# Kernel optimization log

Hardware: AMD Instinct MI355X
Metric: run time of the kernel (lower is better)

## Reference

```python
import jax, jax.numpy as jnp
import numpy as np

D_MODEL = 768
N_HEAD = 12
D_K = D_MODEL // N_HEAD


def setup_inputs() -> dict:
    key = jax.random.key(0)
    ks = jax.random.split(key, 11)
    B, S = 2, 2048
    s = 1.0 / np.sqrt(D_MODEL)
    return {
        "q": jax.random.normal(ks[0], (B, S, D_MODEL), jnp.float32),
        "k": jax.random.normal(ks[1], (B, S, D_MODEL), jnp.float32),
        "v": jax.random.normal(ks[2], (B, S, D_MODEL), jnp.float32),
        "w_q": jax.random.normal(ks[3], (D_MODEL, D_MODEL), jnp.float32) * s,
        "b_q": jnp.zeros((D_MODEL,), jnp.float32),
        "w_k": jax.random.normal(ks[4], (D_MODEL, D_MODEL), jnp.float32) * s,
        "b_k": jnp.zeros((D_MODEL,), jnp.float32),
        "w_v": jax.random.normal(ks[5], (D_MODEL, D_MODEL), jnp.float32) * s,
        "b_v": jnp.zeros((D_MODEL,), jnp.float32),
        "w_o": jax.random.normal(ks[6], (D_MODEL, D_MODEL), jnp.float32) * s,
        "b_o": jnp.zeros((D_MODEL,), jnp.float32),
    }


def reference(q, k, v, w_q, b_q, w_k, b_k, w_v, b_v, w_o, b_o):
    B, S, _ = q.shape
    # QKV projections (nn.Linear: x @ W.T + b)
    Q = q @ w_q.T + b_q
    K = k @ w_k.T + b_k
    V = v @ w_v.T + b_v
    # [B, S, H, d_k] -> [B, H, S, d_k]
    Q = Q.reshape(B, S, N_HEAD, D_K).transpose(0, 2, 1, 3)
    K = K.reshape(B, S, N_HEAD, D_K).transpose(0, 2, 1, 3)
    V = V.reshape(B, S, N_HEAD, D_K).transpose(0, 2, 1, 3)
    # scaled dot-product attention, full [B, H, S, S] scores (as in source)
    scores = jnp.einsum('bhqd,bhkd->bhqk', Q, K) / jnp.sqrt(
        jnp.asarray(D_K, jnp.float32))
    attn = jax.nn.softmax(scores, axis=-1)
    x = jnp.einsum('bhqk,bhkd->bhqd', attn, V)
    x = x.transpose(0, 2, 1, 3).reshape(B, S, D_MODEL)
    out = x @ w_o.T + b_o
    return out, attn
```

## Files before the change

kernel.cpp:

```cpp
#include <hip/hip_runtime.h>

#define DM 768
#define SL 2048
#define NB 2
#define NH 12
#define DK 64

typedef __bf16 bf16x8 __attribute__((ext_vector_type(8)));
typedef float f32x4 __attribute__((ext_vector_type(4)));

__device__ __forceinline__ float bf2f(unsigned short u) {
  return __uint_as_float(((unsigned int)u) << 16);
}
__device__ __forceinline__ unsigned short f2bf(float f) {
  unsigned int u = __float_as_uint(f);
  u += 0x7fff + ((u >> 16) & 1);
  return (unsigned short)(u >> 16);
}

template <int AM, int BM, int OM>
__global__ __launch_bounds__(256) void gemm_bt_t(
    const void* __restrict__ Av, int lda, long sAb, long sAh,
    const void* __restrict__ Bv, int ldb, long sBb, long sBh,
    void* __restrict__ Cv, void* __restrict__ Cv2, int ldc, long sCb, long sCh,
    const float* __restrict__ bias, float scale, int K, int zdiv) {
  constexpr bool SPLIT = (AM == 2);
  const int z = blockIdx.z, zb = z / zdiv, zh = z % zdiv;
  const long aoff = (long)zb * sAb + (long)zh * sAh;
  const long boff = (long)zb * sBb + (long)zh * sBh;
  const long coff = (long)zb * sCb + (long)zh * sCh;
  const int tm = blockIdx.y * 64, tn = blockIdx.x * 64;
  __shared__ __align__(16) unsigned short As[64][40];
  __shared__ __align__(16) unsigned short Bs[64][40];
  __shared__ __align__(16) unsigned short Al[SPLIT ? 64 : 1][40];
  __shared__ __align__(16) unsigned short Bl[SPLIT ? 64 : 1][40];
  const int tid = threadIdx.x;
  const int lrow = tid >> 2, lcol = (tid & 3) * 8;
  const int lane = tid & 63, wave = tid >> 6;
  const int wm = (wave >> 1) * 32, wn = (wave & 1) * 32;
  const int fr = lane & 15, quad = lane >> 4;
  f32x4 acc[2][2] = {};
  for (int k0 = 0; k0 < K; k0 += 32) {
    if constexpr (AM == 0) {
      const unsigned short* Ab = (const unsigned short*)Av + aoff;
      *(uint4*)&As[lrow][lcol] = *(const uint4*)(Ab + (long)(tm + lrow) * lda + k0 + lcol);
    } else {
      const float* Af = (const float*)Av + aoff + (long)(tm + lrow) * lda + k0 + lcol;
      float4 f0 = *(const float4*)Af;
      float4 f1 = *(const float4*)(Af + 4);
      float ff[8] = {f0.x, f0.y, f0.z, f0.w, f1.x, f1.y, f1.z, f1.w};
      unsigned short hi[8];
#pragma unroll
      for (int i = 0; i < 8; ++i) hi[i] = f2bf(ff[i]);
      *(uint4*)&As[lrow][lcol] = *(const uint4*)hi;
      if constexpr (SPLIT) {
        unsigned short lo[8];
#pragma unroll
        for (int i = 0; i < 8; ++i) lo[i] = f2bf(ff[i] - bf2f(hi[i]));
        *(uint4*)&Al[lrow][lcol] = *(const uint4*)lo;
      }
    }
    if constexpr (BM == 0) {
      const unsigned short* Bb = (const unsigned short*)Bv + boff;
      *(uint4*)&Bs[lrow][lcol] = *(const uint4*)(Bb + (long)(tn + lrow) * ldb + k0 + lcol);
    } else {
      const float* Bf = (const float*)Bv + boff + (long)(tn + lrow) * ldb + k0 + lcol;
      float4 f0 = *(const float4*)Bf;
      float4 f1 = *(const float4*)(Bf + 4);
      float ff[8] = {f0.x, f0.y, f0.z, f0.w, f1.x, f1.y, f1.z, f1.w};
      unsigned short hi[8];
#pragma unroll
      for (int i = 0; i < 8; ++i) hi[i] = f2bf(ff[i]);
      *(uint4*)&Bs[lrow][lcol] = *(const uint4*)hi;
      if constexpr (SPLIT) {
        unsigned short lo[8];
#pragma unroll
        for (int i = 0; i < 8; ++i) lo[i] = f2bf(ff[i] - bf2f(hi[i]));
        *(uint4*)&Bl[lrow][lcol] = *(const uint4*)lo;
      }
    }
    __syncthreads();
    bf16x8 a0 = *(const bf16x8*)&As[wm + fr][quad * 8];
    bf16x8 a1 = *(const bf16x8*)&As[wm + 16 + fr][quad * 8];
    bf16x8 b0 = *(const bf16x8*)&Bs[wn + fr][quad * 8];
    bf16x8 b1 = *(const bf16x8*)&Bs[wn + 16 + fr][quad * 8];
    acc[0][0] = __builtin_amdgcn_mfma_f32_16x16x32_bf16(a0, b0, acc[0][0], 0, 0, 0);
    acc[0][1] = __builtin_amdgcn_mfma_f32_16x16x32_bf16(a0, b1, acc[0][1], 0, 0, 0);
    acc[1][0] = __builtin_amdgcn_mfma_f32_16x16x32_bf16(a1, b0, acc[1][0], 0, 0, 0);
    acc[1][1] = __builtin_amdgcn_mfma_f32_16x16x32_bf16(a1, b1, acc[1][1], 0, 0, 0);
    if constexpr (SPLIT) {
      bf16x8 c0 = *(const bf16x8*)&Al[wm + fr][quad * 8];
      bf16x8 c1 = *(const bf16x8*)&Al[wm + 16 + fr][quad * 8];
      bf16x8 d0 = *(const bf16x8*)&Bl[wn + fr][quad * 8];
      bf16x8 d1 = *(const bf16x8*)&Bl[wn + 16 + fr][quad * 8];
      acc[0][0] = __builtin_amdgcn_mfma_f32_16x16x32_bf16(c0, b0, acc[0][0], 0, 0, 0);
      acc[0][1] = __builtin_amdgcn_mfma_f32_16x16x32_bf16(c0, b1, acc[0][1], 0, 0, 0);
      acc[1][0] = __builtin_amdgcn_mfma_f32_16x16x32_bf16(c1, b0, acc[1][0], 0, 0, 0);
      acc[1][1] = __builtin_amdgcn_mfma_f32_16x16x32_bf16(c1, b1, acc[1][1], 0, 0, 0);
      acc[0][0] = __builtin_amdgcn_mfma_f32_16x16x32_bf16(a0, d0, acc[0][0], 0, 0, 0);
      acc[0][1] = __builtin_amdgcn_mfma_f32_16x16x32_bf16(a0, d1, acc[0][1], 0, 0, 0);
      acc[1][0] = __builtin_amdgcn_mfma_f32_16x16x32_bf16(a1, d0, acc[1][0], 0, 0, 0);
      acc[1][1] = __builtin_amdgcn_mfma_f32_16x16x32_bf16(a1, d1, acc[1][1], 0, 0, 0);
    }
    __syncthreads();
  }
#pragma unroll
  for (int sm = 0; sm < 2; ++sm)
#pragma unroll
    for (int sn = 0; sn < 2; ++sn) {
      const int gcol = tn + wn + sn * 16 + fr;
      const float bv = bias ? bias[gcol] : 0.0f;
#pragma unroll
      for (int r = 0; r < 4; ++r) {
        const int grow = tm + wm + sm * 16 + quad * 4 + r;
        const float val = acc[sm][sn][r] * scale + bv;
        const long ci = coff + (long)grow * ldc + gcol;
        if constexpr (OM == 1) {
          ((float*)Cv)[ci] = val;
        } else if constexpr (OM == 0) {
          ((unsigned short*)Cv)[ci] = f2bf(val);
        } else {
          const unsigned short hi = f2bf(val);
          ((unsigned short*)Cv)[ci] = hi;
          ((unsigned short*)Cv2)[ci] = f2bf(val - bf2f(hi));
        }
      }
    }
}

__global__ __launch_bounds__(256) void attn_fused(
    const unsigned short* __restrict__ Qh, const unsigned short* __restrict__ Ql,
    const unsigned short* __restrict__ Kh, const unsigned short* __restrict__ Kl,
    const unsigned short* __restrict__ Vb,
    float* __restrict__ attn, unsigned short* __restrict__ Xb) {
  const int bid = blockIdx.x;
  const int swz = (bid & 7) * 96 + (bid >> 3);
  const int rb = swz & 31;
  const int bh = swz >> 5;
  const int zb = bh / NH, zh = bh - zb * NH;
  const long qoff = (long)zb * SL * DM + zh * DK;
  const unsigned short* Qhb = Qh + qoff;
  const unsigned short* Qlb = Ql + qoff;
  const unsigned short* Khb = Kh + qoff;
  const unsigned short* Klb = Kl + qoff;
  const unsigned short* Vbb = Vb + qoff;
  float* attnb = attn + (long)bh * SL * SL;
  unsigned short* Xbb = Xb + qoff;

  __shared__ __align__(16) unsigned short KhS[64][72];
  __shared__ __align__(16) unsigned short KlS[64][72];
  __shared__ __align__(16) unsigned short VtS[64][72];
  __shared__ __align__(16) float PF[4][16][68];

  const int tid = threadIdx.x;
  const int lane = tid & 63, w = tid >> 6;
  const int fr = lane & 15, quad = lane >> 4;
  const int srow = tid >> 3, scol = (tid & 7) * 8;
  const int row0 = rb * 64 + w * 16;

  bf16x8 qh[2], ql[2];
#pragma unroll
  for (int kc = 0; kc < 2; ++kc) {
    uint4 hv = *(const uint4*)(Qhb + (long)(row0 + fr) * DM + kc * 32 + quad * 8);
    uint4 lv = *(const uint4*)(Qlb + (long)(row0 + fr) * DM + kc * 32 + quad * 8);
    const unsigned short* hp = (const unsigned short*)&hv;
    const unsigned short* lp = (const unsigned short*)&lv;
    unsigned short hs[8], ls[8];
#pragma unroll
    for (int i = 0; i < 8; ++i) {
      hs[i] = f2bf(bf2f(hp[i]) * 0.125f);
      ls[i] = f2bf(bf2f(lp[i]) * 0.125f);
    }
    qh[kc] = *(const bf16x8*)hs;
    ql[kc] = *(const bf16x8*)ls;
  }

  float lsum[4] = {0.0f, 0.0f, 0.0f, 0.0f};

  for (int kt = 0; kt < 32; ++kt) {
#pragma unroll
    for (int hf = 0; hf < 2; ++hf) {
      const int r0 = srow + hf * 32;
      const long g = (long)(kt * 64 + r0) * DM + scol;
      *(uint4*)&KhS[r0][scol] = *(const uint4*)(Khb + g);
      *(uint4*)&KlS[r0][scol] = *(const uint4*)(Klb + g);
    }
    __syncthreads();
    f32x4 s[4] = {};
    __builtin_amdgcn_s_setprio(1);
#pragma unroll
    for (int kc = 0; kc < 2; ++kc)
#pragma unroll
      for (int nf = 0; nf < 4; ++nf) {
        bf16x8 kh_ = *(const bf16x8*)&KhS[nf * 16 + fr][kc * 32 + quad * 8];
        bf16x8 kl_ = *(const bf16x8*)&KlS[nf * 16 + fr][kc * 32 + quad * 8];
        s[nf] = __builtin_amdgcn_mfma_f32_16x16x32_bf16(qh[kc], kh_, s[nf], 0, 0, 0);
        s[nf] = __builtin_amdgcn_mfma_f32_16x16x32_bf16(ql[kc], kh_, s[nf], 0, 0, 0);
        s[nf] = __builtin_amdgcn_mfma_f32_16x16x32_bf16(qh[kc], kl_, s[nf], 0, 0, 0);
      }
    __builtin_amdgcn_s_setprio(0);
#pragma unroll
    for (int nf = 0; nf < 4; ++nf)
#pragma unroll
      for (int r = 0; r < 4; ++r) lsum[r] += __expf(s[nf][r]);
    __syncthreads();
  }
#pragma unroll
  for (int r = 0; r < 4; ++r) {
#pragma unroll
    for (int off = 8; off; off >>= 1) lsum[r] += __shfl_xor(lsum[r], off, 64);
  }
  float inv[4];
#pragma unroll
  for (int r = 0; r < 4; ++r) inv[r] = 1.0f / lsum[r];

  f32x4 o[4] = {};
  for (int kt = 0; kt < 32; ++kt) {
    const int cx = tid & 7;
#pragma unroll
    for (int hf = 0; hf < 2; ++hf) {
      const int r0 = srow + hf * 32;
      const long g = (long)(kt * 64 + r0) * DM + scol;
      *(uint4*)&KhS[r0][scol] = *(const uint4*)(Khb + g);
      *(uint4*)&KlS[r0][scol] = *(const uint4*)(Klb + g);
      uint4 vv = *(const uint4*)(Vbb + g);
      const unsigned short* vp = (const unsigned short*)&vv;
#pragma unroll
      for (int i = 0; i < 8; ++i) {
        const int ii = i ^ (r0 & 7) ^ cx;
        VtS[scol + ii][r0] = vp[ii];
      }
    }
    __syncthreads();
    f32x4 s[4] = {};
    __builtin_amdgcn_s_setprio(1);
#pragma unroll
    for (int kc = 0; kc < 2; ++kc)
#pragma unroll
      for (int nf = 0; nf < 4; ++nf) {
        bf16x8 kh_ = *(const bf16x8*)&KhS[nf * 16 + fr][kc * 32 + quad * 8];
        bf16x8 kl_ = *(const bf16x8*)&KlS[nf * 16 + fr][kc * 32 + quad * 8];
        s[nf] = __builtin_amdgcn_mfma_f32_16x16x32_bf16(qh[kc], kh_, s[nf], 0, 0, 0);
        s[nf] = __builtin_amdgcn_mfma_f32_16x16x32_bf16(ql[kc], kh_, s[nf], 0, 0, 0);
        s[nf] = __builtin_amdgcn_mfma_f32_16x16x32_bf16(qh[kc], kl_, s[nf], 0, 0, 0);
      }
    __builtin_amdgcn_s_setprio(0);
#pragma unroll
    for (int nf = 0; nf < 4; ++nf)
#pragma unroll
      for (int r = 0; r < 4; ++r)
        PF[w][quad * 4 + r][nf * 16 + fr] = __expf(s[nf][r]) * inv[r];
    {
      const int lr = lane >> 2, lc = (lane & 3) * 16;
      float* dst = &attnb[(long)(row0 + lr) * SL + kt * 64 + lc];
      const float* src = &PF[w][lr][lc];
#pragma unroll
      for (int j = 0; j < 4; ++j)
        *(float4*)(dst + j * 4) = *(const float4*)(src + j * 4);
    }
    __builtin_amdgcn_s_setprio(1);
#pragma unroll
    for (int kc = 0; kc < 2; ++kc) {
      const float* pf = &PF[w][fr][kc * 32 + quad * 8];
      float4 p0 = *(const float4*)pf;
      float4 p1 = *(const float4*)(pf + 4);
      union { bf16x8 v; __bf16 e[8]; } pa;
      pa.e[0] = (__bf16)p0.x; pa.e[1] = (__bf16)p0.y;
      pa.e[2] = (__bf16)p0.z; pa.e[3] = (__bf16)p0.w;
      pa.e[4] = (__bf16)p1.x; pa.e[5] = (__bf16)p1.y;
      pa.e[6] = (__bf16)p1.z; pa.e[7] = (__bf16)p1.w;
#pragma unroll
      for (int nf = 0; nf < 4; ++nf) {
        bf16x8 vb_ = *(const bf16x8*)&VtS[nf * 16 + fr][kc * 32 + quad * 8];
        o[nf] = __builtin_amdgcn_mfma_f32_16x16x32_bf16(pa.v, vb_, o[nf], 0, 0, 0);
      }
    }
    __builtin_amdgcn_s_setprio(0);
    __syncthreads();
  }
#pragma unroll
  for (int nf = 0; nf < 4; ++nf)
#pragma unroll
    for (int r = 0; r < 4; ++r)
      Xbb[(long)(row0 + quad * 4 + r) * DM + nf * 16 + fr] = f2bf(o[nf][r]);
}

extern "C" void kernel_launch(void* const* d_in, const int* in_sizes, int n_in,
                              void* d_out, int out_size, void* d_ws, size_t ws_size,
                              hipStream_t stream) {
  const float* q  = (const float*)d_in[0];
  const float* k  = (const float*)d_in[1];
  const float* v  = (const float*)d_in[2];
  const float* wq = (const float*)d_in[3];
  const float* bq = (const float*)d_in[4];
  const float* wk = (const float*)d_in[5];
  const float* bk = (const float*)d_in[6];
  const float* wv = (const float*)d_in[7];
  const float* bv = (const float*)d_in[8];
  const float* wo = (const float*)d_in[9];
  const float* bo = (const float*)d_in[10];

  float* out  = (float*)d_out;
  float* attn = out + (long)NB * SL * DM;

  const long NE = (long)NB * SL * DM;
  unsigned short* Qh = (unsigned short*)d_ws;
  unsigned short* Ql = Qh + NE;
  unsigned short* Kh = Ql + NE;
  unsigned short* Kl = Kh + NE;
  unsigned short* Vbk = Kl + NE;
  unsigned short* Xb = Vbk + NE;

  const dim3 blk(256);
  const dim3 gp(DM / 64, (NB * SL) / 64, 1);

  gemm_bt_t<2, 2, 2><<<gp, blk, 0, stream>>>(q, DM, 0L, 0L, wq, DM, 0L, 0L,
                                             Qh, Ql, DM, 0L, 0L, bq, 1.0f, DM, 1);
  gemm_bt_t<2, 2, 2><<<gp, blk, 0, stream>>>(k, DM, 0L, 0L, wk, DM, 0L, 0L,
                                             Kh, Kl, DM, 0L, 0L, bk, 1.0f, DM, 1);
  gemm_bt_t<1, 1, 0><<<gp, blk, 0, stream>>>(v, DM, 0L, 0L, wv, DM, 0L, 0L,
                                             Vbk, nullptr, DM, 0L, 0L, bv, 1.0f, DM, 1);

  attn_fused<<<dim3((NB * NH * SL) / 64), blk, 0, stream>>>(Qh, Ql, Kh, Kl, Vbk,
                                                            attn, Xb);

  gemm_bt_t<0, 1, 1><<<gp, blk, 0, stream>>>(Xb, DM, 0L, 0L, wo, DM, 0L, 0L,
                                             out, nullptr, DM, 0L, 0L, bo, 1.0f, DM, 1);
}
```

Measured before the change: 716.2 us.

## Compute transposed scores to keep P in registers and drop LDS staging

Swaps the MFMA operand order so each lane holds one query row's scores across keys. Row sums then reduce with two cross-quad shuffles instead of per-row 16-lane reductions. The probability tile no longer round-trips through the PF shared buffer: attn is written directly with float4 stores, and the bf16 A-operand for the PV MFMA is built with packed converts plus permlane swaps. This removes LDS traffic and shared memory use, which may raise occupancy, but relies on gfx950 permlane semantics and changes the global store pattern for attn.

Result: faster. 675.2 us (-5.7%).

```diff
diff --git a/kernel.cpp b/kernel.cpp
--- a/kernel.cpp
+++ b/kernel.cpp
@@ -16,6 +16,11 @@
   unsigned int u = __float_as_uint(f);
   u += 0x7fff + ((u >> 16) & 1);
   return (unsigned short)(u >> 16);
+}
+__device__ __forceinline__ unsigned cvt_pk_bf16(float lo, float hi) {
+  unsigned r;
+  asm("v_cvt_pk_bf16_f32 %0, %1, %2" : "=v"(r) : "v"(lo), "v"(hi));
+  return r;
 }
 
 template <int AM, int BM, int OM>
@@ -150,7 +155,6 @@
   __shared__ __align__(16) unsigned short KhS[64][72];
   __shared__ __align__(16) unsigned short KlS[64][72];
   __shared__ __align__(16) unsigned short VtS[64][72];
-  __shared__ __align__(16) float PF[4][16][68];
 
   const int tid = threadIdx.x;
   const int lane = tid & 63, w = tid >> 6;
@@ -175,7 +179,7 @@
     ql[kc] = *(const bf16x8*)ls;
   }
 
-  float lsum[4] = {0.0f, 0.0f, 0.0f, 0.0f};
+  float lsum = 0.0f;
 
   for (int kt = 0; kt < 32; ++kt) {
 #pragma unroll
@@ -194,25 +198,23 @@
       for (int nf = 0; nf < 4; ++nf) {
         bf16x8 kh_ = *(const bf16x8*)&KhS[nf * 16 + fr][kc * 32 + quad * 8];
         bf16x8 kl_ = *(const bf16x8*)&KlS[nf * 16 + fr][kc * 32 + quad * 8];
-        s[nf] = __builtin_amdgcn_mfma_f32_16x16x32_bf16(qh[kc], kh_, s[nf], 0, 0, 0);
-        s[nf] = __builtin_amdgcn_mfma_f32_16x16x32_bf16(ql[kc], kh_, s[nf], 0, 0, 0);
-        s[nf] = __builtin_amdgcn_mfma_f32_16x16x32_bf16(qh[kc], kl_, s[nf], 0, 0, 0);
+        s[nf] = __builtin_amdgcn_mfma_f32_16x16x32_bf16(kh_, qh[kc], s[nf], 0, 0, 0);
+        s[nf] = __builtin_amdgcn_mfma_f32_16x16x32_bf16(kh_, ql[kc], s[nf], 0, 0, 0);
+        s[nf] = __builtin_amdgcn_mfma_f32_16x16x32_bf16(kl_, qh[kc], s[nf], 0, 0, 0);
       }
     __builtin_amdgcn_s_setprio(0);
-#pragma unroll
-    for (int nf = 0; nf < 4; ++nf)
-#pragma unroll
-      for (int r = 0; r < 4; ++r) lsum[r] += __expf(s[nf][r]);
+    float p0 = 0.0f, p1 = 0.0f, p2 = 0.0f, p3 = 0.0f;
+#pragma unroll
+    for (int nf = 0; nf < 4; ++nf) {
+      p0 += __expf(s[nf][0]); p1 += __expf(s[nf][1]);
+      p2 += __expf(s[nf][2]); p3 += __expf(s[nf][3]);
+    }
+    lsum += (p0 + p1) + (p2 + p3);
     __syncthreads();
   }
-#pragma unroll
-  for (int r = 0; r < 4; ++r) {
-#pragma unroll
-    for (int off = 8; off; off >>= 1) lsum[r] += __shfl_xor(lsum[r], off, 64);
-  }
-  float inv[4];
-#pragma unroll
-  for (int r = 0; r < 4; ++r) inv[r] = 1.0f / lsum[r];
+  lsum += __shfl_xor(lsum, 16, 64);
+  lsum += __shfl_xor(lsum, 32, 64);
+  const float inv = 1.0f / lsum;
 
   f32x4 o[4] = {};
   for (int kt = 0; kt < 32; ++kt) {
@@ -240,42 +242,41 @@
       for (int nf = 0; nf < 4; ++nf) {
         bf16x8 kh_ = *(const bf16x8*)&KhS[nf * 16 + fr][kc * 32 + quad * 8];
         bf16x8 kl_ = *(const bf16x8*)&KlS[nf * 16 + fr][kc * 32 + quad * 8];
-        s[nf] = __builtin_amdgcn_mfma_f32_16x16x32_bf16(qh[kc], kh_, s[nf], 0, 0, 0);
-        s[nf] = __builtin_amdgcn_mfma_f32_16x16x32_bf16(ql[kc], kh_, s[nf], 0, 0, 0);
-        s[nf] = __builtin_amdgcn_mfma_f32_16x16x32_bf16(qh[kc], kl_, s[nf], 0, 0, 0);
+        s[nf] = __builtin_amdgcn_mfma_f32_16x16x32_bf16(kh_, qh[kc], s[nf], 0, 0, 0);
+        s[nf] = __builtin_amdgcn_mfma_f32_16x16x32_bf16(kh_, ql[kc], s[nf], 0, 0, 0);
+        s[nf] = __builtin_amdgcn_mfma_f32_16x16x32_bf16(kl_, qh[kc], s[nf], 0, 0, 0);
       }
     __builtin_amdgcn_s_setprio(0);
+    float p[4][4];
 #pragma unroll
     for (int nf = 0; nf < 4; ++nf)
 #pragma unroll
-      for (int r = 0; r < 4; ++r)
-        PF[w][quad * 4 + r][nf * 16 + fr] = __expf(s[nf][r]) * inv[r];
-    {
-      const int lr = lane >> 2, lc = (lane & 3) * 16;
-      float* dst = &attnb[(long)(row0 + lr) * SL + kt * 64 + lc];
-      const float* src = &PF[w][lr][lc];
-#pragma unroll
-      for (int j = 0; j < 4; ++j)
-        *(float4*)(dst + j * 4) = *(const float4*)(src + j * 4);
-    }
-    __builtin_amdgcn_s_setprio(1);
+      for (int r = 0; r < 4; ++r) p[nf][r] = __expf(s[nf][r]) * inv;
+#pragma unroll
+    for (int nf = 0; nf < 4; ++nf) {
+      float4 st = {p[nf][0], p[nf][1], p[nf][2], p[nf][3]};
+      *(float4*)&attnb[(long)(row0 + fr) * SL + kt * 64 + nf * 16 + quad * 4] = st;
+    }
 #pragma unroll
     for (int kc = 0; kc < 2; ++kc) {
-      const float* pf = &PF[w][fr][kc * 32 + quad * 8];
-      float4 p0 = *(const float4*)pf;
-      float4 p1 = *(const float4*)(pf + 4);
-      union { bf16x8 v; __bf16 e[8]; } pa;
-      pa.e[0] = (__bf16)p0.x; pa.e[1] = (__bf16)p0.y;
-      pa.e[2] = (__bf16)p0.z; pa.e[3] = (__bf16)p0.w;
-      pa.e[4] = (__bf16)p1.x; pa.e[5] = (__bf16)p1.y;
-      pa.e[6] = (__bf16)p1.z; pa.e[7] = (__bf16)p1.w;
+      unsigned x0 = cvt_pk_bf16(p[2 * kc][0], p[2 * kc][1]);
+      unsigned x1 = cvt_pk_bf16(p[2 * kc][2], p[2 * kc][3]);
+      unsigned y0 = cvt_pk_bf16(p[2 * kc + 1][0], p[2 * kc + 1][1]);
+      unsigned y1 = cvt_pk_bf16(p[2 * kc + 1][2], p[2 * kc + 1][3]);
+      asm("v_permlane32_swap_b32 %0, %1" : "+v"(x0), "+v"(y0));
+      asm("v_permlane32_swap_b32 %0, %1" : "+v"(x1), "+v"(y1));
+      asm("v_permlane16_swap_b32 %0, %1" : "+v"(x0), "+v"(y0));
+      asm("v_permlane16_swap_b32 %0, %1" : "+v"(x1), "+v"(y1));
+      union { unsigned u[4]; bf16x8 v; } pa;
+      pa.u[0] = x0; pa.u[1] = x1; pa.u[2] = y0; pa.u[3] = y1;
+      __builtin_amdgcn_s_setprio(1);
 #pragma unroll
       for (int nf = 0; nf < 4; ++nf) {
         bf16x8 vb_ = *(const bf16x8*)&VtS[nf * 16 + fr][kc * 32 + quad * 8];
         o[nf] = __builtin_amdgcn_mfma_f32_16x16x32_bf16(pa.v, vb_, o[nf], 0, 0, 0);
       }
-    }
-    __builtin_amdgcn_s_setprio(0);
+      __builtin_amdgcn_s_setprio(0);
+    }
     __syncthreads();
   }
 #pragma unroll
```
